# Performance work log

Measured on AMD Instinct MI355X. Metric: run time of the kernel, lower is better.

## Reference

```python
import jax, jax.numpy as jnp
import numpy as np

N_PRED = 10000
N_GT = 1000
NUM_CLASSES = 80
IMG_H = 800
IMG_W = 1333
EPS = 1e-12
ALPHA, GAMMA, CLS_W = 0.25, 2.0, 2.0
L1_W, IOU_W = 5.0, 2.0
CENTER_RADIUS = 2.5
CAND_TOPK = 5


def _make_boxes(key, n, w, h):
    k1, k2 = jax.random.split(key)
    cxcy = jax.random.uniform(k1, (n, 2)) * jnp.array([w, h], jnp.float32)
    wh = jax.random.uniform(k2, (n, 2)) * 190.0 + 10.0
    return jnp.concatenate([cxcy - wh / 2, cxcy + wh / 2], axis=1).astype(jnp.float32)


def setup_inputs() -> dict:
    key = jax.random.key(0)
    k1, k2, k3, k4 = jax.random.split(key, 4)
    return {
        'pred_logits': jax.random.normal(k1, (N_PRED, NUM_CLASSES), jnp.float32),
        'pred_boxes': _make_boxes(k2, N_PRED, IMG_W, IMG_H),
        'gt_bboxes': _make_boxes(k3, N_GT, IMG_W, IMG_H),
        'gt_labels': jax.random.randint(k4, (N_GT,), 0, NUM_CLASSES),
        'img_h': IMG_H,
        'img_w': IMG_W,
    }


def _pairwise_iou_giou(pred, gt):
    area_p = (pred[:, 2] - pred[:, 0]) * (pred[:, 3] - pred[:, 1])
    area_g = (gt[:, 2] - gt[:, 0]) * (gt[:, 3] - gt[:, 1])
    lt = jnp.maximum(pred[:, None, :2], gt[None, :, :2])
    rb = jnp.minimum(pred[:, None, 2:], gt[None, :, 2:])
    wh = jnp.clip(rb - lt, 0.0)
    inter = wh[..., 0] * wh[..., 1]                       # [N,G]
    union = area_p[:, None] + area_g[None, :] - inter
    iou = inter / jnp.maximum(union, EPS)
    elt = jnp.minimum(pred[:, None, :2], gt[None, :, :2])
    erb = jnp.maximum(pred[:, None, 2:], gt[None, :, 2:])
    ewh = jnp.clip(erb - elt, 0.0)
    enclose = ewh[..., 0] * ewh[..., 1]
    giou = iou - (enclose - union) / jnp.maximum(enclose, EPS)
    return iou, giou


def _center_info(pred, gt):
    # pred/gt in xyxy; uses pred box centers, strict inequalities as in source
    pcx = (pred[:, 0] + pred[:, 2]) * 0.5
    pcy = (pred[:, 1] + pred[:, 3]) * 0.5
    gx1, gy1, gx2, gy2 = gt[:, 0], gt[:, 1], gt[:, 2], gt[:, 3]
    in_boxes = ((pcx[:, None] > gx1) & (pcx[:, None] < gx2) &
                (pcy[:, None] > gy1) & (pcy[:, None] < gy2))
    gcx, gcy = (gx1 + gx2) * 0.5, (gy1 + gy2) * 0.5
    gw, gh = gx2 - gx1, gy2 - gy1
    r = CENTER_RADIUS
    in_centers = ((pcx[:, None] > gcx - r * gw) & (pcx[:, None] < gcx + r * gw) &
                  (pcy[:, None] > gcy - r * gh) & (pcy[:, None] < gcy + r * gh))
    valid = in_boxes.any(1) | in_centers.any(1)
    return valid, in_boxes & in_centers


def _compute_cost_and_ious(pred_logits, pred_boxes, gt_bboxes, gt_labels, img_h, img_w):
    # FocalLossCost
    p = jax.nn.sigmoid(pred_logits)
    neg = -jnp.log1p(-(p - EPS)) * (1 - ALPHA) * p ** GAMMA
    pos = -jnp.log(p + EPS) * ALPHA * (1 - p) ** GAMMA
    cls_cost = (pos - neg)[:, gt_labels] * CLS_W            # [N,G]
    # BBoxL1Cost (normalized by image size)
    factor = jnp.array([img_w, img_h, img_w, img_h], jnp.float32)
    l1_cost = jnp.sum(jnp.abs(pred_boxes[:, None, :] / factor -
                              gt_bboxes[None, :, :] / factor), -1) * L1_W
    # IoUCost (giou) + pairwise ious for dynamic-k
    ious, giou = _pairwise_iou_giou(pred_boxes, gt_bboxes)
    iou_cost = -giou * IOU_W
    valid_mask, in_boxes_and_center = _center_info(pred_boxes, gt_bboxes)
    cost = cls_cost + l1_cost + iou_cost + jnp.where(in_boxes_and_center, 0.0, 100.0)
    cost = cost + jnp.where(valid_mask, 0.0, 10000.0)[:, None]
    return cost, ious


def _dynamic_k_matching(cost, ious):
    n, g = cost.shape
    k = min(CAND_TOPK, n)
    topk_ious, _ = jax.lax.top_k(ious.T, k)                 # [G,k]
    dynamic_ks = jnp.maximum(topk_ious.sum(1).astype(jnp.int32), 1)
    _, idx = jax.lax.top_k(-cost.T, k)                      # [G,k] smallest costs per gt
    vals = (jnp.arange(k)[None, :] < dynamic_ks[:, None]).astype(cost.dtype)
    cols = jnp.broadcast_to(jnp.arange(g)[:, None], (g, k))
    mm = jnp.zeros_like(cost).at[idx, cols].max(vals)       # scatter 1s per gt column
    # resolve priors matched to >1 gt (note: mask is reused stale inside the loop, as in source)
    prior_mask = mm.sum(1) > 1
    cmin = jnp.argmin(cost, axis=1)
    mm = jnp.where(prior_mask[:, None], jax.nn.one_hot(cmin, g, dtype=cost.dtype), mm)

    def cond(state):
        m, _ = state
        return jnp.any(m.sum(0) == 0)

    def body(state):
        m, c = state
        matched_q = m.sum(1) > 0
        c = c + 100000.0 * matched_q[:, None].astype(c.dtype)
        unmatched = m.sum(0) == 0
        pos = jnp.argmin(c, axis=0)                         # [G]
        oh = jax.nn.one_hot(pos, n, dtype=c.dtype).T        # [N,G]
        m = jnp.where(unmatched[None, :], oh, m)
        cmin2 = jnp.argmin(c, axis=1)
        m_fix = jnp.where(prior_mask[:, None], jax.nn.one_hot(cmin2, g, dtype=c.dtype), m)
        m = jnp.where(jnp.any(m.sum(1) > 1), m_fix, m)
        return (m, c)

    mm, _ = jax.lax.while_loop(cond, body, (mm, cost))
    fg_mask = mm.sum(1) > 0
    matched = jnp.argmax(mm, axis=1).astype(jnp.int32)
    return fg_mask, jnp.where(fg_mask, matched, 0)


def reference(pred_logits, pred_boxes, gt_bboxes, gt_labels, img_h, img_w):
    cost, ious = _compute_cost_and_ious(pred_logits, pred_boxes, gt_bboxes,
                                        gt_labels, img_h, img_w)
    fg_mask, matched_gt = _dynamic_k_matching(cost, ious)
    # dense form: matched_gt[i] valid only where fg_mask[i] (fixed-shape version of
    # the original's compressed matched_gt_inds = mm[fg_mask].argmax(1))
    return fg_mask, matched_gt
```

## Files before the change

kernel.cpp:

```cpp
#include <hip/hip_runtime.h>
#include <cfloat>
#include <cmath>

#define NP 10000
#define NG 1000
#define NC 80
#define LMAX 6
#define NCH 2
#define CHSZ (NP / NCH)
#define MAIN_IT 19
#define TAIL_N  136

#define S_MULTI 12
#define S_BODY  16
#define RI_BIG  0x3fffffff
#define KMAX    0xFFFFFFFFFFFFFFFFull

__device__ __forceinline__ bool lexless(float av, int ai, float bv, int bi) {
    return (av < bv) || (av == bv && ai < bi);
}

__device__ __forceinline__ unsigned long long packkey(float v, int idx) {
    unsigned u = __float_as_uint(v);
    u ^= (unsigned)(((int)u) >> 31) | 0x80000000u;
    return ((unsigned long long)u << 32) | (unsigned)idx;
}
__device__ __forceinline__ int keyidx(unsigned long long k) {
    return (int)(unsigned)(k & 0xFFFFFFFFu);
}

__device__ __forceinline__ float inflate(float c, int k) {
    for (int q = 0; q < k; q++) c += 100000.0f;
    return c;
}

__device__ __forceinline__ void cost_iou(float4 p, float4 pn, float4 pi,
        float4 g, float4 cb, float4 Gn, float ga, float clsv,
        float& cc_out, float& iou_out) {
#pragma clang fp contract(off)
    float wx = fminf(p.z, g.z) - fmaxf(p.x, g.x); wx = fmaxf(wx, 0.0f);
    float wy = fminf(p.w, g.w) - fmaxf(p.y, g.y); wy = fmaxf(wy, 0.0f);
    float inter = wx * wy;
    float uni = pi.z + ga - inter;
    float iou = inter / fmaxf(uni, 1e-12f);
    float ex = fmaxf(p.z, g.z) - fminf(p.x, g.x); ex = fmaxf(ex, 0.0f);
    float ey = fmaxf(p.w, g.w) - fminf(p.y, g.y); ey = fmaxf(ey, 0.0f);
    float enc = ex * ey;
    float giou = iou - (enc - uni) / fmaxf(enc, 1e-12f);
    float l1 = ((fabsf(pn.x - Gn.x) + fabsf(pn.y - Gn.y))
                + fabsf(pn.z - Gn.z)) + fabsf(pn.w - Gn.w);
    float cc = clsv + l1 * 5.0f;
    cc = cc + (-giou * 2.0f);
    bool inb = (pi.x > g.x && pi.x < g.z && pi.y > g.y && pi.y < g.w);
    bool inc = (pi.x > cb.x && pi.x < cb.z && pi.y > cb.y && pi.y < cb.w);
    cc = cc + ((inb && inc) ? 0.0f : 100.0f);
    cc = cc + pi.w;
    cc_out = cc; iou_out = iou;
}

#define CLS_TI 64
#define PB_CLS0 40
#define PB_G0   197
#define PB_V0   201
__global__ __launch_bounds__(256) void k_prep(const float* __restrict__ logits,
        const float* __restrict__ pb, const float* __restrict__ gb,
        const int* __restrict__ imgw, const int* __restrict__ imgh,
        float* __restrict__ clsval, float4* __restrict__ pnorm,
        float4* __restrict__ pinfo, float4* __restrict__ gcb,
        float4* __restrict__ gnm, float* __restrict__ gar,
        int* rowcnt, int* rowfirst, int* rowiter, int* prior, int* priorcol,
        int* colsum, int* scal)
{
    __shared__ float sl[CLS_TI * (NC + 1)];
    int b = blockIdx.x;
    if (b < PB_CLS0) {
        int i = b * 256 + threadIdx.x;
        if (i < NP) {
            rowcnt[i] = 0; rowfirst[i] = 0x7fffffff; rowiter[i] = RI_BIG;
            prior[i] = 0; priorcol[i] = 0;
        }
        if (i < NG) colsum[i] = 0;
        if (i < 32) scal[i] = 0;
    } else if (b < PB_G0) {
        int i0 = (b - PB_CLS0) * CLS_TI;
        bool full = (i0 + CLS_TI) <= NP;
        if (full) {
            const float* src = logits + (size_t)i0 * NC;
            for (int e = threadIdx.x; e < CLS_TI * NC; e += 256) {
                int di = e / NC, c = e - di * NC;
                sl[di * (NC + 1) + c] = src[e];
            }
        } else {
            for (int e = threadIdx.x; e < CLS_TI * NC; e += 256) {
                int di = e / NC, c = e - di * NC;
                int i = i0 + di;
                sl[di * (NC + 1) + c] = (i < NP) ? logits[(size_t)i * NC + c] : 0.0f;
            }
        }
        __syncthreads();
        for (int e = threadIdx.x; e < CLS_TI * NC; e += 256) {
            int c = e >> 6, di = e & 63;
            int i = i0 + di;
            if (i >= NP) continue;
            float x = sl[di * (NC + 1) + c];
            float p = 1.0f / (1.0f + expf(-x));
            float neg = -log1pf(-(p - 1e-12f)) * 0.75f * (p * p);
            float om = 1.0f - p;
            float pos = -logf(p + 1e-12f) * 0.25f * (om * om);
            clsval[(size_t)c * NP + i] = (pos - neg) * 2.0f;
        }
    } else if (b < PB_V0) {
#pragma clang fp contract(off)
        int j = (b - PB_G0) * 256 + threadIdx.x;
        if (j < NG) {
            float fw = (float)imgw[0], fh = (float)imgh[0];
            float4 g = ((const float4*)gb)[j];
            float gcx = (g.x + g.z) * 0.5f, gcy = (g.y + g.w) * 0.5f;
            float gw = g.z - g.x, gh = g.w - g.y;
            float4 cb; cb.x = gcx - 2.5f * gw; cb.y = gcy - 2.5f * gh;
            cb.z = gcx + 2.5f * gw; cb.w = gcy + 2.5f * gh;
            gcb[j] = cb;
            float4 Gn; Gn.x = g.x / fw; Gn.y = g.y / fh; Gn.z = g.z / fw; Gn.w = g.w / fh;
            gnm[j] = Gn;
            gar[j] = (g.z - g.x) * (g.w - g.y);
        }
    } else {
#pragma clang fp contract(off)
        int wave = threadIdx.x >> 6;
        int lane = threadIdx.x & 63;
        int i = (b - PB_V0) * 4 + wave;
        if (i >= NP) return;
        float4 p = ((const float4*)pb)[i];
        float pcx = (p.x + p.z) * 0.5f, pcy = (p.y + p.w) * 0.5f;
        int vb = 0, vc = 0;
        const float4* gb4 = (const float4*)gb;
        for (int j = lane; j < NG; j += 64) {
            float4 g = gb4[j];
            vb |= (pcx > g.x && pcx < g.z && pcy > g.y && pcy < g.w) ? 1 : 0;
            float gcx = (g.x + g.z) * 0.5f, gcy = (g.y + g.w) * 0.5f;
            float gw = g.z - g.x, gh = g.w - g.y;
            vc |= (pcx > gcx - 2.5f * gw && pcx < gcx + 2.5f * gw &&
                   pcy > gcy - 2.5f * gh && pcy < gcy + 2.5f * gh) ? 1 : 0;
        }
        int any = (__any(vb) ? 1 : 0) | (__any(vc) ? 1 : 0);
        if (lane == 0) {
            float fw = (float)imgw[0], fh = (float)imgh[0];
            float4 pn; pn.x = p.x / fw; pn.y = p.y / fh; pn.z = p.z / fw; pn.w = p.w / fh;
            pnorm[i] = pn;
            float4 pi4; pi4.x = pcx; pi4.y = pcy;
            pi4.z = (p.z - p.x) * (p.w - p.y);
            pi4.w = any ? 0.0f : 10000.0f;
            pinfo[i] = pi4;
        }
    }
}

__device__ __forceinline__ void upd2(unsigned long long& k0,
        unsigned long long& k1, unsigned long long key) {
    unsigned long long mx = (k0 > key) ? k0 : key;
    k0 = (k0 > key) ? key : k0;
    k1 = (k1 > mx) ? mx : k1;
}
__device__ __forceinline__ void updi2(float& i0, float& i1, float iou) {
    float mnv = fminf(i0, iou);
    i0 = fmaxf(i0, iou);
    i1 = fmaxf(i1, mnv);
}

__global__ __launch_bounds__(256) void k_cost2(
        const float* __restrict__ pb, const float* __restrict__ gb,
        const int* __restrict__ glab, const float* __restrict__ clsval,
        const float4* __restrict__ pnorm, const float4* __restrict__ pinfo,
        const float4* __restrict__ gcb, const float4* __restrict__ gnm,
        const float* __restrict__ gar,
        unsigned long long* __restrict__ pck, float* __restrict__ piv)
{
    __shared__ unsigned long long s_k[256 * 7];
    __shared__ float s_iv[256 * 7];
    __shared__ int s_bad;

    int j = blockIdx.x >> 1;
    int c = blockIdx.x & 1;
    int tid = threadIdx.x;
    if (tid == 0) s_bad = 0;
    float4 g  = ((const float4*)gb)[j];
    float4 cb = gcb[j];
    float4 Gn = gnm[j];
    float  ga = gar[j];
    const float* clscol = clsval + (size_t)glab[j] * NP;
    const float4* pb4 = (const float4*)pb;
    int base_i = c * CHSZ;

    unsigned long long k0a = KMAX, k1a = KMAX, k0b = KMAX, k1b = KMAX;
    float i0a = -1.0f, i1a = -1.0f, i0b = -1.0f, i1b = -1.0f;
#pragma unroll 2
    for (int k = 0; k + 1 < MAIN_IT; k += 2) {
        int ia = base_i + tid + k * 256;
        int ib = ia + 256;
        float cca, ioua, ccb, ioub;
        cost_iou(pb4[ia], pnorm[ia], pinfo[ia], g, cb, Gn, ga, clscol[ia], cca, ioua);
        cost_iou(pb4[ib], pnorm[ib], pinfo[ib], g, cb, Gn, ga, clscol[ib], ccb, ioub);
        upd2(k0a, k1a, packkey(cca, ia));
        upd2(k0b, k1b, packkey(ccb, ib));
        updi2(i0a, i1a, ioua);
        updi2(i0b, i1b, ioub);
    }
    {
        int i = base_i + tid + (MAIN_IT - 1) * 256;
        float cc, iou;
        cost_iou(pb4[i], pnorm[i], pinfo[i], g, cb, Gn, ga, clscol[i], cc, iou);
        upd2(k0a, k1a, packkey(cc, i));
        updi2(i0a, i1a, iou);
    }
    if (tid < TAIL_N) {
        int i = base_i + MAIN_IT * 256 + tid;
        float cc, iou;
        cost_iou(pb4[i], pnorm[i], pinfo[i], g, cb, Gn, ga, clscol[i], cc, iou);
        upd2(k0b, k1b, packkey(cc, i));
        updi2(i0b, i1b, iou);
    }

    unsigned long long m0 = (k0a < k0b) ? k0a : k0b;
    unsigned long long x1 = (k0a < k0b) ? k0b : k0a;
    unsigned long long x2 = (k1a < k1b) ? k1a : k1b;
    unsigned long long m3 = (k1a < k1b) ? k1b : k1a;
    unsigned long long m1 = (x1 < x2) ? x1 : x2;
    unsigned long long m2 = (x1 < x2) ? x2 : x1;
    float n0 = fmaxf(i0a, i0b);
    float y1 = fminf(i0a, i0b);
    float y2 = fmaxf(i1a, i1b);
    float n3 = fminf(i1a, i1b);
    float n1 = fmaxf(y1, y2);
    float n2 = fminf(y1, y2);

    int base = tid * 7;
    s_k[base+0] = m0; s_k[base+1] = m1; s_k[base+2] = m2; s_k[base+3] = m3;
    s_k[base+4] = KMAX; s_k[base+5] = KMAX;
    s_iv[base+0] = n0; s_iv[base+1] = n1; s_iv[base+2] = n2; s_iv[base+3] = n3;
    s_iv[base+4] = -2.0f; s_iv[base+5] = -2.0f;
    __syncthreads();

    for (int w = 128; w > 0; w >>= 1) {
        if (tid < w) {
            int a = tid * 7, bb = (tid + w) * 7;
            unsigned long long ok[5]; float og[5];
            int pa = a, pbp = bb;
#pragma unroll
            for (int t = 0; t < 5; t++) {
                unsigned long long A = s_k[pa], B = s_k[pbp];
                if (A <= B) { ok[t] = A; pa++; } else { ok[t] = B; pbp++; }
            }
            int qa = a, qb = bb;
#pragma unroll
            for (int t = 0; t < 5; t++) {
                float A = s_iv[qa], B = s_iv[qb];
                if (A >= B) { og[t] = A; qa++; } else { og[t] = B; qb++; }
            }
#pragma unroll
            for (int t = 0; t < 5; t++) { s_k[a+t] = ok[t]; s_iv[a+t] = og[t]; }
        }
        __syncthreads();
    }

    if (k1a < s_k[4] || k1b < s_k[4] || i1a > s_iv[4] || i1b > s_iv[4]) s_bad = 1;
    __syncthreads();

    if (s_bad) {
        unsigned long long kv[5]; float iv[5];
#pragma unroll
        for (int t = 0; t < 5; t++) { kv[t] = KMAX; iv[t] = -1.0f; }
        for (int k = 0; k <= MAIN_IT; k++) {
            if (k == MAIN_IT && tid >= TAIL_N) break;
            int i = base_i + tid + k * 256;
            float cc, iou;
            cost_iou(pb4[i], pnorm[i], pinfo[i], g, cb, Gn, ga, clscol[i], cc, iou);
            unsigned long long key = packkey(cc, i);
            if (key < kv[4]) {
                kv[4] = key;
#pragma unroll
                for (int t = 4; t > 0; t--)
                    if (kv[t] < kv[t-1]) { unsigned long long tv = kv[t]; kv[t] = kv[t-1]; kv[t-1] = tv; }
            }
            if (iou > iv[4]) {
                iv[4] = iou;
#pragma unroll
                for (int t = 4; t > 0; t--)
                    if (iv[t] > iv[t-1]) { float tv = iv[t]; iv[t] = iv[t-1]; iv[t-1] = tv; }
            }
        }
#pragma unroll
        for (int t = 0; t < 5; t++) { s_k[base+t] = kv[t]; s_iv[base+t] = iv[t]; }
        s_k[base+5] = KMAX; s_iv[base+5] = -2.0f;
        __syncthreads();
        for (int w = 128; w > 0; w >>= 1) {
            if (tid < w) {
                int a = tid * 7, bb = (tid + w) * 7;
                unsigned long long ok[5]; float og[5];
                int pa = a, pbp = bb;
#pragma unroll
                for (int t = 0; t < 5; t++) {
                    unsigned long long A = s_k[pa], B = s_k[pbp];
                    if (A <= B) { ok[t] = A; pa++; } else { ok[t] = B; pbp++; }
                }
                int qa = a, qb = bb;
#pragma unroll
                for (int t = 0; t < 5; t++) {
                    float A = s_iv[qa], B = s_iv[qb];
                    if (A >= B) { og[t] = A; qa++; } else { og[t] = B; qb++; }
                }
#pragma unroll
                for (int t = 0; t < 5; t++) { s_k[a+t] = ok[t]; s_iv[a+t] = og[t]; }
            }
            __syncthreads();
        }
    }

    if (tid == 0) {
        int ob = blockIdx.x * 5;
#pragma unroll
        for (int t = 0; t < 5; t++) { pck[ob + t] = s_k[t]; piv[ob + t] = s_iv[t]; }
    }
}

__global__ __launch_bounds__(256) void k_costmerge(
        const unsigned long long* __restrict__ pck, const float* __restrict__ piv,
        int* __restrict__ rowcnt, int* __restrict__ rowfirst,
        int* __restrict__ rowiter, int* __restrict__ top5,
        int* __restrict__ dkarr)
{
    int j = blockIdx.x * 256 + threadIdx.x;
    if (j >= NG) return;
    int base = j * 2 * 5;
    int h0 = 0, h1 = 0;
    int besti[5];
#pragma unroll
    for (int r = 0; r < 5; r++) {
        unsigned long long v0 = pck[base + h0];
        unsigned long long v1 = pck[base + 5 + h1];
        if (v0 <= v1) { besti[r] = keyidx(v0); h0++; }
        else          { besti[r] = keyidx(v1); h1++; }
    }
    int g0 = 0, g1 = 0;
    float ivm[5];
#pragma unroll
    for (int r = 0; r < 5; r++) {
        float v0 = piv[base + g0];
        float v1 = piv[base + 5 + g1];
        if (v0 >= v1) { ivm[r] = v0; g0++; } else { ivm[r] = v1; g1++; }
    }
    float s = (((ivm[0] + ivm[1]) + ivm[2]) + ivm[3]) + ivm[4];
    int dk = (int)s;
    if (dk < 1) dk = 1;
    dkarr[j] = dk;
#pragma unroll
    for (int r = 0; r < 5; r++) top5[j * 5 + r] = besti[r];
    for (int t = 0; t < dk; t++) {
        int r = besti[t];
        atomicAdd(&rowcnt[r], 1);
        atomicMin(&rowfirst[r], j);
        atomicMin(&rowiter[r], -1);
    }
}

__global__ __launch_bounds__(256) void k_pfixsurv(const float* __restrict__ pb,
        const float* __restrict__ gb, const int* __restrict__ glab,
        const float* __restrict__ clsval,
        const float4* __restrict__ pnorm, const float4* __restrict__ pinfo,
        const float4* __restrict__ gcb, const float4* __restrict__ gnm,
        const float* __restrict__ gar,
        int* __restrict__ prior, int* __restrict__ priorcol,
        int* __restrict__ colsum,
        const int* __restrict__ rowcnt, const int* __restrict__ top5,
        const int* __restrict__ dkarr)
{
    int b = blockIdx.x;
    int tid = threadIdx.x;
    if (b >= 2500) {
        int j = (b - 2500) * 256 + tid;
        if (j >= NG) return;
        int c = 0;
        int dk = dkarr[j];
        for (int t = 0; t < dk; t++) if (rowcnt[top5[j * 5 + t]] == 1) c++;
        if (c) atomicAdd(&colsum[j], c);
        return;
    }
    __shared__ float rv[256]; __shared__ int ri[256];
    for (int q = 0; q < 4; q++) {
        int row = b * 4 + q;
        if (rowcnt[row] <= 1) continue;
        if (tid == 0) prior[row] = 1;
        float4 p = ((const float4*)pb)[row];
        float4 pn = pnorm[row];
        float4 pi4 = pinfo[row];
        float best = FLT_MAX; int bj = 0x7fffffff;
        for (int j = tid; j < NG; j += 256) {
            float cc, iou;
            cost_iou(p, pn, pi4, ((const float4*)gb)[j], gcb[j], gnm[j], gar[j],
                     clsval[(size_t)glab[j] * NP + row], cc, iou);
            if (lexless(cc, j, best, bj)) { best = cc; bj = j; }
        }
        rv[tid] = best; ri[tid] = bj; __syncthreads();
        for (int w = 128; w > 0; w >>= 1) {
            if (tid < w) {
                float ov = rv[tid + w]; int oi = ri[tid + w];
                if (lexless(ov, oi, rv[tid], ri[tid])) { rv[tid] = ov; ri[tid] = oi; }
            }
            __syncthreads();
        }
        if (tid == 0) {
            priorcol[row] = ri[0];
            atomicAdd(&colsum[ri[0]], 1);
        }
        __syncthreads();
    }
}

__global__ __launch_bounds__(256) void k_iterB(const float* __restrict__ pb,
        const float* __restrict__ gb, const int* __restrict__ glab,
        const float* __restrict__ clsval,
        const float4* __restrict__ pnorm, const float4* __restrict__ pinfo,
        const float4* __restrict__ gcb, const float4* __restrict__ gnm,
        const float* __restrict__ gar, const int* __restrict__ top5,
        int* __restrict__ rowiter, int* __restrict__ rowcnt,
        int* __restrict__ rowfirst, int* __restrict__ colsum,
        int* __restrict__ scal, int t)
{
    int j = blockIdx.x;
    if (colsum[j] != 0) return;
    int tid = threadIdx.x;
    if (tid == 0) scal[S_BODY + t] = 1;

    __shared__ int s_pos;
    if (tid == 0) {
        int pos = -1;
        for (int r = 0; r < 5; r++) {
            int i = top5[j * 5 + r];
            if (rowiter[i] >= t) { pos = i; break; }
        }
        s_pos = pos;
    }
    __syncthreads();
    int pos = s_pos;

    if (pos < 0) {
        float4 g  = ((const float4*)gb)[j];
        float4 cb = gcb[j];
        float4 Gn = gnm[j];
        float  ga = gar[j];
        const float* clscol = clsval + (size_t)glab[j] * NP;
        const float4* pb4 = (const float4*)pb;
        __shared__ float rv[256]; __shared__ int ri[256];
        float best = FLT_MAX; int bi = 0x7fffffff;
        for (int i = tid; i < NP; i += 256) {
            if (rowiter[i] < t) continue;
            float cc, iou;
            cost_iou(pb4[i], pnorm[i], pinfo[i], g, cb, Gn, ga, clscol[i], cc, iou);
            if (lexless(cc, i, best, bi)) { best = cc; bi = i; }
        }
        rv[tid] = best; ri[tid] = bi; __syncthreads();
        for (int w = 128; w > 0; w >>= 1) {
            if (tid < w) {
                float ov = rv[tid + w]; int oi = ri[tid + w];
                if (lexless(ov, oi, rv[tid], ri[tid])) { rv[tid] = ov; ri[tid] = oi; }
            }
            __syncthreads();
        }
        pos = ri[0];
    }

    if (tid == 0) {
        colsum[j] = 1;
        int old = atomicAdd(&rowcnt[pos], 1);
        if (old >= 1) scal[S_MULTI] = 1;
        atomicMin(&rowfirst[pos], j);
        atomicMin(&rowiter[pos], t);
    }
}

__global__ __launch_bounds__(256) void k_iterC(const float* __restrict__ pb,
        const float* __restrict__ gb, const int* __restrict__ glab,
        const float* __restrict__ clsval,
        const float4* __restrict__ pnorm, const float4* __restrict__ pinfo,
        const float4* __restrict__ gcb, const float4* __restrict__ gnm,
        const float* __restrict__ gar,
        const int* __restrict__ prior, const int* __restrict__ rowiter,
        int* __restrict__ priorcol, int* __restrict__ colsum,
        int* __restrict__ scal, int t)
{
    if (scal[S_BODY + t] == 0 || scal[S_MULTI] == 0) return;
    int b = blockIdx.x;
    int tid = threadIdx.x;
    __shared__ float rv[256]; __shared__ int ri[256];
    for (int q = 0; q < 4; q++) {
        int row = b * 4 + q;
        if (!prior[row]) continue;
        int k = t - rowiter[row]; if (k < 0) k = 0;
        float4 p = ((const float4*)pb)[row];
        float4 pn = pnorm[row];
        float4 pi4 = pinfo[row];
        float best = FLT_MAX; int bj = 0x7fffffff;
        for (int j = tid; j < NG; j += 256) {
            float cc, iou;
            cost_iou(p, pn, pi4, ((const float4*)gb)[j], gcb[j], gnm[j], gar[j],
                     clsval[(size_t)glab[j] * NP + row], cc, iou);
            float val = inflate(cc, k);
            if (lexless(val, j, best, bj)) { best = val; bj = j; }
        }
        rv[tid] = best; ri[tid] = bj; __syncthreads();
        for (int w = 128; w > 0; w >>= 1) {
            if (tid < w) {
                float ov = rv[tid + w]; int oi = ri[tid + w];
                if (lexless(ov, oi, rv[tid], ri[tid])) { rv[tid] = ov; ri[tid] = oi; }
            }
            __syncthreads();
        }
        if (tid == 0) {
            int nb = ri[0];
            int oldc = priorcol[row];
            if (nb != oldc) {
                atomicSub(&colsum[oldc], 1);
                atomicAdd(&colsum[nb], 1);
                priorcol[row] = nb;
            }
        }
        __syncthreads();
    }
}

__global__ __launch_bounds__(256) void k_final(const int* __restrict__ rowcnt,
        const int* __restrict__ prior, const int* __restrict__ priorcol,
        const int* __restrict__ rowfirst, int* __restrict__ out)
{
    int i = blockIdx.x * 256 + threadIdx.x;
    if (i >= NP) return;
    int fg = rowcnt[i] > 0;
    out[i] = fg ? 1 : 0;
    out[NP + i] = fg ? (prior[i] ? priorcol[i] : rowfirst[i]) : 0;
}

extern "C" void kernel_launch(void* const* d_in, const int* in_sizes, int n_in,
                              void* d_out, int out_size, void* d_ws, size_t ws_size,
                              hipStream_t stream)
{
    (void)in_sizes; (void)n_in; (void)out_size; (void)ws_size;
    const float* logits = (const float*)d_in[0];
    const float* pboxes = (const float*)d_in[1];
    const float* gboxes = (const float*)d_in[2];
    const int*   glab   = (const int*)d_in[3];
    const int*   imgh   = (const int*)d_in[4];
    const int*   imgw   = (const int*)d_in[5];
    int* out = (int*)d_out;

    char* w = (char*)d_ws;
    float*  clsval  = (float*)(w);
    float4* pnorm   = (float4*)(w + 3200000);
    float4* pinfo   = (float4*)(w + 3360000);
    float4* gcb     = (float4*)(w + 3520000);
    float4* gnm     = (float4*)(w + 3536000);
    float*  gar     = (float*)(w + 3552000);
    int* rowcnt     = (int*)(w + 3556000);
    int* rowfirst   = (int*)(w + 3596000);
    int* rowiter    = (int*)(w + 3636000);
    int* prior      = (int*)(w + 3676000);
    int* priorcol   = (int*)(w + 3716000);
    int* top5       = (int*)(w + 3756000);
    int* dkarr      = (int*)(w + 3776000);
    int* colsum     = (int*)(w + 3780000);
    int* scal       = (int*)(w + 3784000);
    unsigned long long* pck = (unsigned long long*)(w + 3784128);
    float* piv      = (float*)(w + 3864128);

    hipLaunchKernelGGL(k_prep, dim3(2701), dim3(256), 0, stream,
                       logits, pboxes, gboxes, imgw, imgh,
                       clsval, pnorm, pinfo, gcb, gnm, gar,
                       rowcnt, rowfirst, rowiter, prior, priorcol, colsum, scal);
    hipLaunchKernelGGL(k_cost2, dim3(NG * NCH), dim3(256), 0, stream,
                       pboxes, gboxes, glab, clsval, pnorm, pinfo, gcb, gnm, gar,
                       pck, piv);
    hipLaunchKernelGGL(k_costmerge, dim3(4), dim3(256), 0, stream,
                       pck, piv, rowcnt, rowfirst, rowiter, top5, dkarr);
    hipLaunchKernelGGL(k_pfixsurv, dim3(2504), dim3(256), 0, stream,
                       pboxes, gboxes, glab, clsval, pnorm, pinfo, gcb, gnm, gar,
                       prior, priorcol, colsum, rowcnt, top5, dkarr);
    for (int t = 0; t < LMAX; t++) {
        hipLaunchKernelGGL(k_iterB, dim3(NG), dim3(256), 0, stream,
                           pboxes, gboxes, glab, clsval, pnorm, pinfo, gcb, gnm, gar,
                           top5, rowiter, rowcnt, rowfirst, colsum, scal, t);
        hipLaunchKernelGGL(k_iterC, dim3(2500), dim3(256), 0, stream,
                           pboxes, gboxes, glab, clsval, pnorm, pinfo, gcb, gnm, gar,
                           prior, rowiter, priorcol, colsum, scal, t);
    }
    hipLaunchKernelGGL(k_final, dim3(40), dim3(256), 0, stream,
                       rowcnt, prior, priorcol, rowfirst, out);
}
```

Before: 164.0 us.

## Compact overlapping candidates before cost evaluation and early-exit the center prefilter

In the cost kernel, each block first runs a cheap box-overlap test over its prediction chunk and compacts the overlapping indices into a shared-memory list with ballot and atomic add. The full cost/IoU evaluation and top-k tracking then run only on that list. Non-overlapping predictions are handled by a threshold key check that falls back to the full recompute path when too few candidates exist or the list overflows. Separately, the prefilter loop over GT boxes now exits once any lane in the wave has found a hit. Together these aim to skip most of the per-pair cost math, at the price of extra synchronizations and a possible fallback that redoes the full scan.

```diff
diff --git a/kernel.cpp b/kernel.cpp
--- a/kernel.cpp
+++ b/kernel.cpp
@@ -15,6 +15,9 @@
 #define S_BODY  16
 #define RI_BIG  0x3fffffff
 #define KMAX    0xFFFFFFFFFFFFFFFFull
+
+#define TKEY    0xC248000000000000ull
+#define CAND_CAP 1536
 
 __device__ __forceinline__ bool lexless(float av, int ai, float bv, int bi) {
     return (av < bv) || (av == bv && ai < bi);
@@ -134,15 +137,19 @@
         float pcx = (p.x + p.z) * 0.5f, pcy = (p.y + p.w) * 0.5f;
         int vb = 0, vc = 0;
         const float4* gb4 = (const float4*)gb;
-        for (int j = lane; j < NG; j += 64) {
-            float4 g = gb4[j];
-            vb |= (pcx > g.x && pcx < g.z && pcy > g.y && pcy < g.w) ? 1 : 0;
-            float gcx = (g.x + g.z) * 0.5f, gcy = (g.y + g.w) * 0.5f;
-            float gw = g.z - g.x, gh = g.w - g.y;
-            vc |= (pcx > gcx - 2.5f * gw && pcx < gcx + 2.5f * gw &&
-                   pcy > gcy - 2.5f * gh && pcy < gcy + 2.5f * gh) ? 1 : 0;
-        }
-        int any = (__any(vb) ? 1 : 0) | (__any(vc) ? 1 : 0);
+        for (int jb = 0; jb < NG; jb += 64) {
+            int j = jb + lane;
+            if (j < NG) {
+                float4 g = gb4[j];
+                vb |= (pcx > g.x && pcx < g.z && pcy > g.y && pcy < g.w) ? 1 : 0;
+                float gcx = (g.x + g.z) * 0.5f, gcy = (g.y + g.w) * 0.5f;
+                float gw = g.z - g.x, gh = g.w - g.y;
+                vc |= (pcx > gcx - 2.5f * gw && pcx < gcx + 2.5f * gw &&
+                       pcy > gcy - 2.5f * gh && pcy < gcy + 2.5f * gh) ? 1 : 0;
+            }
+            if (__any(vb | vc)) break;
+        }
+        int any = __any(vb | vc) ? 1 : 0;
         if (lane == 0) {
             float fw = (float)imgw[0], fh = (float)imgh[0];
             float4 pn; pn.x = p.x / fw; pn.y = p.y / fh; pn.z = p.z / fw; pn.w = p.w / fh;
@@ -178,11 +185,13 @@
     __shared__ unsigned long long s_k[256 * 7];
     __shared__ float s_iv[256 * 7];
     __shared__ int s_bad;
+    __shared__ int s_cnt;
+    int* s_list = (int*)s_iv;
 
     int j = blockIdx.x >> 1;
     int c = blockIdx.x & 1;
     int tid = threadIdx.x;
-    if (tid == 0) s_bad = 0;
+    if (tid == 0) { s_bad = 0; s_cnt = 0; }
     float4 g  = ((const float4*)gb)[j];
     float4 cb = gcb[j];
     float4 Gn = gnm[j];
@@ -190,54 +199,46 @@
     const float* clscol = clsval + (size_t)glab[j] * NP;
     const float4* pb4 = (const float4*)pb;
     int base_i = c * CHSZ;
-
-    unsigned long long k0a = KMAX, k1a = KMAX, k0b = KMAX, k1b = KMAX;
-    float i0a = -1.0f, i1a = -1.0f, i0b = -1.0f, i1b = -1.0f;
-#pragma unroll 2
-    for (int k = 0; k + 1 < MAIN_IT; k += 2) {
-        int ia = base_i + tid + k * 256;
-        int ib = ia + 256;
-        float cca, ioua, ccb, ioub;
-        cost_iou(pb4[ia], pnorm[ia], pinfo[ia], g, cb, Gn, ga, clscol[ia], cca, ioua);
-        cost_iou(pb4[ib], pnorm[ib], pinfo[ib], g, cb, Gn, ga, clscol[ib], ccb, ioub);
-        upd2(k0a, k1a, packkey(cca, ia));
-        upd2(k0b, k1b, packkey(ccb, ib));
-        updi2(i0a, i1a, ioua);
-        updi2(i0b, i1b, ioub);
-    }
-    {
-        int i = base_i + tid + (MAIN_IT - 1) * 256;
+    __syncthreads();
+
+    for (int k = 0; k <= MAIN_IT; k++) {
+        if (k == MAIN_IT && tid >= TAIL_N) break;
+        int i = base_i + tid + k * 256;
+        float4 p = pb4[i];
+        bool o = (p.z > g.x) & (g.z > p.x) & (p.w > g.y) & (g.w > p.y);
+        unsigned long long m = __ballot(o ? 1 : 0);
+        if (m) {
+            int ln = tid & 63;
+            int basew = 0;
+            if (ln == 0) basew = atomicAdd(&s_cnt, __popcll(m));
+            basew = __shfl(basew, 0);
+            if (o) {
+                int slot = basew + __popcll(m & ((1ull << ln) - 1ull));
+                if (slot < CAND_CAP) s_list[slot] = i;
+            }
+        }
+    }
+    __syncthreads();
+    int cnt = s_cnt;
+    bool overflow = (cnt > CAND_CAP);
+    if (overflow) cnt = 0;
+
+    unsigned long long k0 = KMAX, k1 = KMAX;
+    float i0 = 0.0f, i1 = 0.0f;
+    for (int q = tid; q < cnt; q += 256) {
+        int i = s_list[q];
         float cc, iou;
         cost_iou(pb4[i], pnorm[i], pinfo[i], g, cb, Gn, ga, clscol[i], cc, iou);
-        upd2(k0a, k1a, packkey(cc, i));
-        updi2(i0a, i1a, iou);
-    }
-    if (tid < TAIL_N) {
-        int i = base_i + MAIN_IT * 256 + tid;
-        float cc, iou;
-        cost_iou(pb4[i], pnorm[i], pinfo[i], g, cb, Gn, ga, clscol[i], cc, iou);
-        upd2(k0b, k1b, packkey(cc, i));
-        updi2(i0b, i1b, iou);
-    }
-
-    unsigned long long m0 = (k0a < k0b) ? k0a : k0b;
-    unsigned long long x1 = (k0a < k0b) ? k0b : k0a;
-    unsigned long long x2 = (k1a < k1b) ? k1a : k1b;
-    unsigned long long m3 = (k1a < k1b) ? k1b : k1a;
-    unsigned long long m1 = (x1 < x2) ? x1 : x2;
-    unsigned long long m2 = (x1 < x2) ? x2 : x1;
-    float n0 = fmaxf(i0a, i0b);
-    float y1 = fminf(i0a, i0b);
-    float y2 = fmaxf(i1a, i1b);
-    float n3 = fminf(i1a, i1b);
-    float n1 = fmaxf(y1, y2);
-    float n2 = fminf(y1, y2);
+        upd2(k0, k1, packkey(cc, i));
+        updi2(i0, i1, iou);
+    }
+    __syncthreads();
 
     int base = tid * 7;
-    s_k[base+0] = m0; s_k[base+1] = m1; s_k[base+2] = m2; s_k[base+3] = m3;
-    s_k[base+4] = KMAX; s_k[base+5] = KMAX;
-    s_iv[base+0] = n0; s_iv[base+1] = n1; s_iv[base+2] = n2; s_iv[base+3] = n3;
-    s_iv[base+4] = -2.0f; s_iv[base+5] = -2.0f;
+    s_k[base+0] = k0; s_k[base+1] = k1;
+    s_k[base+2] = KMAX; s_k[base+3] = KMAX; s_k[base+4] = KMAX; s_k[base+5] = KMAX;
+    s_iv[base+0] = i0; s_iv[base+1] = i1;
+    s_iv[base+2] = 0.0f; s_iv[base+3] = 0.0f; s_iv[base+4] = 0.0f; s_iv[base+5] = 0.0f;
     __syncthreads();
 
     for (int w = 128; w > 0; w >>= 1) {
@@ -262,7 +263,7 @@
         __syncthreads();
     }
 
-    if (k1a < s_k[4] || k1b < s_k[4] || i1a > s_iv[4] || i1b > s_iv[4]) s_bad = 1;
+    if (overflow || s_k[4] >= TKEY || k1 < s_k[4] || i1 > s_iv[4]) s_bad = 1;
     __syncthreads();
 
     if (s_bad) {
```

After: 158.7 us. 3.3% less time.
